# Optimization experiments

Hardware: AMD Instinct MI355X
Metric: run time of the kernel (lower is better)

The kernel has to match this reference:

```python
import jax, jax.numpy as jnp
import numpy as np

GN_GROUPS = 32
GN_EPS = 1e-5


def conv1x1(x, w, b):
    # x: [B,C,H,W], w: [O,C], b: [O]
    return jnp.einsum('bchw,oc->bohw', x, w) + b[None, :, None, None]


def maxpool2(x):
    B, C, H, W = x.shape
    return x.reshape(B, C, H // 2, 2, W // 2, 2).max(axis=(3, 5))


def group_norm(x, w, b, groups=GN_GROUPS, eps=GN_EPS):
    B, C, H, W = x.shape
    xg = x.reshape(B, groups, -1)
    m = xg.mean(axis=-1, keepdims=True)
    v = xg.var(axis=-1, keepdims=True)
    xn = ((xg - m) * jax.lax.rsqrt(v + eps)).reshape(B, C, H, W)
    return xn * w[None, :, None, None] + b[None, :, None, None]


def setup_inputs() -> dict:
    key = jax.random.key(0)
    ks = jax.random.split(key, 8)
    B, C, Ci, H, W = 4, 128, 64, 96, 96
    s_in = 1.0 / np.sqrt(C)
    s_ic = 1.0 / np.sqrt(Ci)
    return {
        'x': jax.random.normal(ks[0], (B, C, H, W), jnp.float32),
        'w_theta': jax.random.normal(ks[1], (Ci, C), jnp.float32) * s_in,
        'b_theta': jnp.zeros((Ci,), jnp.float32),
        'w_phi': jax.random.normal(ks[2], (Ci, C), jnp.float32) * s_in,
        'b_phi': jnp.zeros((Ci,), jnp.float32),
        'w_g': jax.random.normal(ks[3], (Ci, C), jnp.float32) * s_in,
        'b_g': jnp.zeros((Ci,), jnp.float32),
        'w_W': jax.random.normal(ks[4], (C, Ci), jnp.float32) * s_ic,
        'b_W': jnp.zeros((C,), jnp.float32),
        'gn_w': jnp.ones((C,), jnp.float32),
        'gn_b': jnp.zeros((C,), jnp.float32),
    }


def reference(x, w_theta, b_theta, w_phi, b_phi, w_g, b_g, w_W, b_W, gn_w, gn_b):
    B, C, H, W = x.shape
    Ci = w_theta.shape[0]
    # projections (1x1 convs); phi and g are 2x2 max-pooled (sub_sample=True)
    theta = conv1x1(x, w_theta, b_theta).reshape(B, Ci, H * W)          # [B,Ci,N]
    phi = maxpool2(conv1x1(x, w_phi, b_phi)).reshape(B, Ci, -1)         # [B,Ci,N']
    g = maxpool2(conv1x1(x, w_g, b_g)).reshape(B, Ci, -1)               # [B,Ci,N']
    # unscaled single-head attention
    f = jnp.einsum('bcn,bcm->bnm', theta, phi)                          # [B,N,N']
    f = jax.nn.softmax(f, axis=-1)
    y = jnp.einsum('bnm,bcm->bcn', f, g).reshape(B, Ci, H, W)           # [B,Ci,H,W]
    w_y = group_norm(conv1x1(y, w_W, b_W), gn_w, gn_b)
    return w_y + x
```

## Files before the change

kernel.cpp:

```cpp
#include <hip/hip_runtime.h>
#include <math.h>

#define B_ 4
#define C_ 128
#define CI_ 64
#define H_ 96
#define W_ 96
#define HW_ (H_*W_)
#define NP_ 2304
#define GROUPS_ 32
#define EPS_ 1e-5f
#define KVT_ 32
#define NT_ (NP_/KVT_)

typedef _Float16 f16x8 __attribute__((ext_vector_type(8)));
typedef _Float16 f16x2 __attribute__((ext_vector_type(2)));
typedef __attribute__((ext_vector_type(4))) float f32x4;

__device__ inline f32x4 mfma16h(f16x8 a, f16x8 b, f32x4 c) {
    return __builtin_amdgcn_mfma_f32_16x16x32_f16(a, b, c, 0, 0, 0);
}
__device__ inline float h2f(unsigned short s) {
    return (float)__builtin_bit_cast(_Float16, s);
}
__device__ inline unsigned pk_f16(float a, float b) {
    return __builtin_bit_cast(unsigned, __builtin_amdgcn_cvt_pkrtz(a, b));
}
__device__ inline f16x8 pk8(float v0, float v1, float v2, float v3,
                            float v4, float v5, float v6, float v7) {
    uint4 u = { pk_f16(v0, v1), pk_f16(v2, v3), pk_f16(v4, v5), pk_f16(v6, v7) };
    return __builtin_bit_cast(f16x8, u);
}
__device__ inline void gload_lds16(const void* g, void* l) {
    __builtin_amdgcn_global_load_lds(
        (const __attribute__((address_space(1))) void*)reinterpret_cast<uintptr_t>(g),
        (__attribute__((address_space(3))) void*)(unsigned)reinterpret_cast<uintptr_t>(l),
        16, 0, 0);
}

__global__ __launch_bounds__(256) void wprep_kernel(
    const float* __restrict__ w_theta, const float* __restrict__ w_phi,
    const float* __restrict__ w_g,     const float* __restrict__ w_W,
    unsigned short* __restrict__ Whall)
{
    const int idx = blockIdx.x * 256 + threadIdx.x;
    float v;
    if      (idx <  8192) v = w_theta[idx];
    else if (idx < 16384) v = w_phi[idx - 8192];
    else if (idx < 24576) v = w_g[idx - 16384];
    else                  v = w_W[idx - 24576];
    Whall[idx] = __builtin_bit_cast(unsigned short, (_Float16)v);
}

__global__ __launch_bounds__(256) void proj_kernel(
    const float* __restrict__ x, const unsigned short* __restrict__ Whall,
    const float* __restrict__ b_theta, const float* __restrict__ b_phi,
    const float* __restrict__ b_g,
    unsigned short* __restrict__ Qo, unsigned short* __restrict__ phiF,
    unsigned short* __restrict__ gF)
{
    __shared__ __align__(16) unsigned short pb[4][16 * 72];

    const int t    = threadIdx.x;
    const int wv   = t >> 6;
    const int lane = t & 63;
    const int lr   = lane & 15;
    const int lg   = lane >> 4;
    const int b    = blockIdx.y;
    const int px0  = blockIdx.x * 64 + wv * 16;

    const float* xb = x + (size_t)b * C_ * HW_ + px0 + lr;
    f16x8 xa[4];
    #pragma unroll
    for (int u = 0; u < 4; ++u) {
        const float* p = xb + (size_t)(u * 32 + lg * 8) * HW_;
        xa[u] = pk8(p[0], p[(size_t)HW_], p[2 * (size_t)HW_], p[3 * (size_t)HW_],
                    p[4 * (size_t)HW_], p[5 * (size_t)HW_], p[6 * (size_t)HW_],
                    p[7 * (size_t)HW_]);
    }

    #pragma unroll
    for (int mat = 0; mat < 3; ++mat) {
        const unsigned short* Whp = Whall + mat * 8192;
        const float* bsel = (mat == 0) ? b_theta : (mat == 1) ? b_phi : b_g;
        unsigned short* osel = (mat == 0) ? Qo : (mat == 1) ? phiF : gF;

        f32x4 D[4];
        #pragma unroll
        for (int ct = 0; ct < 4; ++ct) D[ct] = (f32x4){0.f, 0.f, 0.f, 0.f};
        #pragma unroll
        for (int u = 0; u < 4; ++u)
            #pragma unroll
            for (int ct = 0; ct < 4; ++ct) {
                f16x8 wb = *(const f16x8*)&Whp[(ct * 16 + lr) * 128 + u * 32 + lg * 8];
                D[ct] = mfma16h(xa[u], wb, D[ct]);
            }

        #pragma unroll
        for (int ct = 0; ct < 4; ++ct) {
            const float bi = bsel[ct * 16 + lr];
            #pragma unroll
            for (int r2 = 0; r2 < 4; ++r2)
                pb[wv][(4 * lg + r2) * 72 + ct * 16 + lr] =
                    __builtin_bit_cast(unsigned short, (_Float16)(D[ct][r2] + bi));
        }
        {
            const int px = lane >> 2, ch = lane & 3;
            f16x8 y0 = *(const f16x8*)&pb[wv][px * 72 + ch * 16];
            f16x8 y1 = *(const f16x8*)&pb[wv][px * 72 + ch * 16 + 8];
            unsigned short* op = osel + ((size_t)b * HW_ + px0 + px) * CI_ + ch * 16;
            *(f16x8*)op       = y0;
            *(f16x8*)(op + 8) = y1;
        }
    }
}

__global__ __launch_bounds__(256) void pool_kernel(
    const unsigned short* __restrict__ phiF, const unsigned short* __restrict__ gF,
    unsigned short* __restrict__ Ko, unsigned short* __restrict__ Vt)
{
    const int t   = threadIdx.x;
    const int b   = blockIdx.y;
    const int mat = blockIdx.z;
    const int idx = blockIdx.x * 256 + t;
    int m, ci;
    if (mat == 0) { m = idx >> 6; ci = idx & 63; }
    else          { ci = idx / NP_; m = idx - ci * NP_; }
    const int ph = m / 48, pw = m % 48;
    const int n00 = (ph * 2) * W_ + pw * 2;
    const unsigned short* src = mat ? gF : phiF;
    const unsigned short* p = src + ((size_t)b * HW_ + n00) * CI_ + ci;
    float v = fmaxf(fmaxf(h2f(p[0]), h2f(p[CI_])),
                    fmaxf(h2f(p[(size_t)W_ * CI_]), h2f(p[(size_t)(W_ + 1) * CI_])));
    unsigned short r = __builtin_bit_cast(unsigned short, (_Float16)v);
    if (mat == 0) {
        Ko[((size_t)b * NP_ + m) * CI_ + ci] = r;
    } else {
        const int ms = (m & ~31) | (8 * ((m >> 2) & 3) + 4 * ((m >> 4) & 1) + (m & 3));
        Vt[((size_t)b * CI_ + ci) * NP_ + ms] = r;
    }
}

__global__ __launch_bounds__(128) void attn_kernel(
    const unsigned short* __restrict__ Qg, const unsigned short* __restrict__ Kg,
    const unsigned short* __restrict__ Vt, unsigned short* __restrict__ Yh)
{
    __shared__ unsigned char Klds[2][4096];
    __shared__ unsigned char Vlds[2][4096];

    const int t    = threadIdx.x;
    const int wv   = t >> 6;
    const int lane = t & 63;
    const int lr   = lane & 15;
    const int lg   = lane >> 4;
    const int b    = blockIdx.y;
    const int q0   = blockIdx.x * 32 + wv * 16;

    const int krow = lane >> 3;
    const int kchk = (lane & 7) ^ krow;
    const int vrow = lane >> 2;
    const int vchk = (lane & 3) ^ (vrow & 3);

    const unsigned short* Kb = Kg + (size_t)b * NP_ * CI_;
    const unsigned short* Vb = Vt + (size_t)b * CI_ * NP_;

    f16x8 qf[2];
    #pragma unroll
    for (int u = 0; u < 2; ++u)
        qf[u] = *(const f16x8*)(Qg + ((size_t)b * HW_ + q0 + lr) * CI_ + u * 32 + lg * 8);

    f32x4 o_acc[4];
    #pragma unroll
    for (int dt = 0; dt < 4; ++dt) o_acc[dt] = (f32x4){0.f, 0.f, 0.f, 0.f};
    float mrun = -1e30f, lrun = 0.f;

#define STAGE(BUF, TT)                                                          \
    {                                                                           \
        const int kv0_ = (TT) * KVT_;                                           \
        if (wv == 0) {                                                          \
            _Pragma("unroll")                                                   \
            for (int i = 0; i < 4; ++i)                                         \
                gload_lds16(Kb + (size_t)(kv0_ + 8 * i + krow) * CI_ + kchk * 8,\
                            &Klds[BUF][i * 1024]);                              \
        } else {                                                                \
            _Pragma("unroll")                                                   \
            for (int i = 0; i < 4; ++i)                                         \
                gload_lds16(Vb + (size_t)(16 * i + vrow) * NP_ + kv0_ + vchk * 8,\
                            &Vlds[BUF][i * 1024]);                              \
        }                                                                       \
    }

#define COMPUTE(BUF)                                                            \
    {                                                                           \
        f16x8 kf[2][2];                                                         \
        _Pragma("unroll")                                                       \
        for (int u = 0; u < 2; ++u)                                             \
            _Pragma("unroll")                                                   \
            for (int k4 = 0; k4 < 2; ++k4)                                      \
                kf[u][k4] = *(const f16x8*)&Klds[BUF][(k4 * 16 + lr) * 128      \
                                + (((4 * u + lg) ^ (lr & 7)) << 4)];            \
        f32x4 s[2];                                                             \
        s[0] = (f32x4){0.f, 0.f, 0.f, 0.f};                                     \
        s[1] = (f32x4){0.f, 0.f, 0.f, 0.f};                                     \
        __builtin_amdgcn_s_setprio(1);                                          \
        _Pragma("unroll")                                                       \
        for (int u = 0; u < 2; ++u) {                                           \
            s[0] = mfma16h(kf[u][0], qf[u], s[0]);                              \
            s[1] = mfma16h(kf[u][1], qf[u], s[1]);                              \
        }                                                                       \
        __builtin_amdgcn_s_setprio(0);                                          \
        float tmax = fmaxf(fmaxf(fmaxf(s[0][0], s[0][1]),                       \
                                 fmaxf(s[0][2], s[0][3])),                      \
                           fmaxf(fmaxf(s[1][0], s[1][1]),                       \
                                 fmaxf(s[1][2], s[1][3])));                     \
        if (!__all(tmax <= mrun + 8.0f)) {                                      \
            tmax = fmaxf(tmax, __shfl_xor(tmax, 16));                           \
            tmax = fmaxf(tmax, __shfl_xor(tmax, 32));                           \
            const float mnew = fmaxf(mrun, tmax);                               \
            const float sc = __expf(mrun - mnew);                               \
            lrun *= sc;                                                         \
            _Pragma("unroll")                                                   \
            for (int r2 = 0; r2 < 4; ++r2) {                                    \
                const float scb = __shfl(sc, 4 * lg + r2);                      \
                _Pragma("unroll")                                               \
                for (int dt = 0; dt < 4; ++dt) o_acc[dt][r2] *= scb;            \
            }                                                                   \
            mrun = mnew;                                                        \
        }                                                                       \
        const float e00 = __expf(s[0][0] - mrun);                               \
        const float e01 = __expf(s[0][1] - mrun);                               \
        const float e02 = __expf(s[0][2] - mrun);                               \
        const float e03 = __expf(s[0][3] - mrun);                               \
        const float e10 = __expf(s[1][0] - mrun);                               \
        const float e11 = __expf(s[1][1] - mrun);                               \
        const float e12 = __expf(s[1][2] - mrun);                               \
        const float e13 = __expf(s[1][3] - mrun);                               \
        lrun += ((e00 + e01) + (e02 + e03)) + ((e10 + e11) + (e12 + e13));      \
        f16x8 pf = pk8(e00, e01, e02, e03, e10, e11, e12, e13);                 \
        __builtin_amdgcn_s_setprio(1);                                          \
        _Pragma("unroll")                                                       \
        for (int dt = 0; dt < 4; ++dt) {                                        \
            const int vrow_ = dt * 16 + lr;                                     \
            f16x8 vf = *(const f16x8*)&Vlds[BUF][vrow_ * 64                     \
                            + (((lg ^ (lr & 3))) << 4)];                        \
            o_acc[dt] = mfma16h(pf, vf, o_acc[dt]);                             \
        }                                                                       \
        __builtin_amdgcn_s_setprio(0);                                          \
    }

    STAGE(0, 0);
    STAGE(1, 1);

    for (int it = 0; it < NT_ / 2; ++it) {
        const int t0 = 2 * it;
        asm volatile("s_waitcnt vmcnt(4)" ::: "memory");
        __builtin_amdgcn_s_barrier();
        COMPUTE(0);
        __builtin_amdgcn_s_barrier();
        if (t0 + 2 < NT_) STAGE(0, t0 + 2);
        if (it == NT_ / 2 - 1) {
            asm volatile("s_waitcnt vmcnt(0)" ::: "memory");
        } else {
            asm volatile("s_waitcnt vmcnt(4)" ::: "memory");
        }
        __builtin_amdgcn_s_barrier();
        COMPUTE(1);
        __builtin_amdgcn_s_barrier();
        if (t0 + 3 < NT_) STAGE(1, t0 + 3);
    }

    float lt = lrun;
    lt += __shfl_xor(lt, 16);
    lt += __shfl_xor(lt, 32);
    unsigned short* yb = (unsigned short*)&Klds[wv][0];
    #pragma unroll
    for (int r2 = 0; r2 < 4; ++r2) {
        const float inv = 1.0f / __shfl(lt, 4 * lg + r2);
        #pragma unroll
        for (int dt = 0; dt < 4; ++dt)
            yb[(4 * lg + r2) * 72 + dt * 16 + lr] =
                __builtin_bit_cast(unsigned short, (_Float16)(o_acc[dt][r2] * inv));
    }
    {
        const int px = lane >> 2, ch = lane & 3;
        f16x8 y0 = *(const f16x8*)&yb[px * 72 + ch * 16];
        f16x8 y1 = *(const f16x8*)&yb[px * 72 + ch * 16 + 8];
        unsigned short* op = Yh + ((size_t)b * HW_ + q0 + px) * CI_ + ch * 16;
        *(f16x8*)op       = y0;
        *(f16x8*)(op + 8) = y1;
    }
#undef STAGE
#undef COMPUTE
}

__global__ __launch_bounds__(256) void conv2_kernel(
    const unsigned short* __restrict__ Yh, const unsigned short* __restrict__ wWh,
    const float* __restrict__ bW, float* __restrict__ Zg, float* __restrict__ gpart)
{
    __shared__ float wpart[4][32][2];

    const int t    = threadIdx.x;
    const int wv   = t >> 6;
    const int lane = t & 63;
    const int lr   = lane & 15;
    const int lg   = lane >> 4;
    const int b    = blockIdx.y;
    const int n0   = blockIdx.x * 64 + wv * 16;

    f16x8 ya[2];
    #pragma unroll
    for (int u = 0; u < 2; ++u)
        ya[u] = *(const f16x8*)(Yh + ((size_t)b * HW_ + n0 + lr) * CI_ + u * 32 + lg * 8);

    float* Zb = Zg + (size_t)b * C_ * HW_ + n0 + lr;
    #pragma unroll
    for (int ot = 0; ot < 8; ++ot) {
        f32x4 D = (f32x4){0.f, 0.f, 0.f, 0.f};
        #pragma unroll
        for (int u = 0; u < 2; ++u) {
            f16x8 wa = *(const f16x8*)&wWh[(ot * 16 + lr) * CI_ + u * 32 + lg * 8];
            D = mfma16h(wa, ya[u], D);
        }
        float zs = 0.f, zq = 0.f;
        #pragma unroll
        for (int r2 = 0; r2 < 4; ++r2) {
            const int o = ot * 16 + 4 * lg + r2;
            const float z = D[r2] + bW[o];
            Zb[(size_t)o * HW_] = z;
            zs += z;
            zq += z * z;
        }
        zs += __shfl_xor(zs, 1);  zq += __shfl_xor(zq, 1);
        zs += __shfl_xor(zs, 2);  zq += __shfl_xor(zq, 2);
        zs += __shfl_xor(zs, 4);  zq += __shfl_xor(zq, 4);
        zs += __shfl_xor(zs, 8);  zq += __shfl_xor(zq, 8);
        if (lr == 0) {
            wpart[wv][ot * 4 + lg][0] = zs;
            wpart[wv][ot * 4 + lg][1] = zq;
        }
    }
    __syncthreads();
    if (t < 64) {
        const int g = t >> 1, w = t & 1;
        const float v = wpart[0][g][w] + wpart[1][g][w]
                      + wpart[2][g][w] + wpart[3][g][w];
        gpart[(((size_t)b * 144 + blockIdx.x) * 32 + g) * 2 + w] = v;
    }
}

__global__ __launch_bounds__(256) void final_kernel(
    const float* __restrict__ Zg, const float* __restrict__ xg,
    const float* __restrict__ gpart, const float* __restrict__ gnw,
    const float* __restrict__ gnb, float* __restrict__ out)
{
    __shared__ float red[256][2];
    const int t = threadIdx.x;
    const int c = blockIdx.x;
    const int b = blockIdx.y;
    const int g = c >> 2;

    float v1 = 0.f, v2 = 0.f;
    if (t < 144) {
        v1 = gpart[(((size_t)b * 144 + t) * 32 + g) * 2 + 0];
        v2 = gpart[(((size_t)b * 144 + t) * 32 + g) * 2 + 1];
    }
    red[t][0] = v1; red[t][1] = v2;
    __syncthreads();
    for (int off = 128; off > 0; off >>= 1) {
        if (t < off) { red[t][0] += red[t + off][0]; red[t][1] += red[t + off][1]; }
        __syncthreads();
    }
    const float invn = 1.0f / (4 * HW_);
    const float mean = red[0][0] * invn;
    const float var  = red[0][1] * invn - mean * mean;
    const float rstd = rsqrtf(var + EPS_);
    const float sc = rstd * gnw[c];
    const float sh = gnb[c] - mean * sc;

    const float4* zp = (const float4*)(Zg + ((size_t)b * C_ + c) * HW_);
    const float4* xp = (const float4*)(xg + ((size_t)b * C_ + c) * HW_);
    float4*       op = (float4*)(out + ((size_t)b * C_ + c) * HW_);
    #pragma unroll
    for (int i = 0; i < HW_ / 4 / 256; ++i) {
        const int j = i * 256 + t;
        const float4 z  = zp[j];
        const float4 xv = xp[j];
        float4 o;
        o.x = z.x * sc + sh + xv.x;
        o.y = z.y * sc + sh + xv.y;
        o.z = z.z * sc + sh + xv.z;
        o.w = z.w * sc + sh + xv.w;
        op[j] = o;
    }
}

extern "C" void kernel_launch(void* const* d_in, const int* in_sizes, int n_in,
                              void* d_out, int out_size, void* d_ws, size_t ws_size,
                              hipStream_t stream)
{
    const float* x       = (const float*)d_in[0];
    const float* w_theta = (const float*)d_in[1];
    const float* b_theta = (const float*)d_in[2];
    const float* w_phi   = (const float*)d_in[3];
    const float* b_phi   = (const float*)d_in[4];
    const float* w_g     = (const float*)d_in[5];
    const float* b_g     = (const float*)d_in[6];
    const float* w_W     = (const float*)d_in[7];
    const float* b_W     = (const float*)d_in[8];
    const float* gn_w    = (const float*)d_in[9];
    const float* gn_b    = (const float*)d_in[10];
    float* out = (float*)d_out;
    char* wsb  = (char*)d_ws;

    unsigned short* Q    = (unsigned short*)(wsb);
    unsigned short* K    = (unsigned short*)(wsb +  4718592);
    unsigned short* Vt   = (unsigned short*)(wsb +  5898240);
    unsigned short* phiF = (unsigned short*)(wsb +  7077888);
    unsigned short* gF   = (unsigned short*)(wsb + 11796480);
    unsigned short* Yh   = (unsigned short*)(wsb +  7077888);
    float* gpart         = (float*)(wsb + 11796480);
    float* Z             = (float*)(wsb + 16515072);
    unsigned short* Whall= (unsigned short*)(wsb + 35390464);
    unsigned short* wWh  = Whall + 24576;

    wprep_kernel<<<128, 256, 0, stream>>>(w_theta, w_phi, w_g, w_W, Whall);
    proj_kernel <<<dim3(HW_ / 64, B_), 256, 0, stream>>>(
        x, Whall, b_theta, b_phi, b_g, Q, phiF, gF);
    pool_kernel <<<dim3(NP_ * CI_ / 256, B_, 2), 256, 0, stream>>>(phiF, gF, K, Vt);
    attn_kernel <<<dim3(HW_ / 32, B_), 128, 0, stream>>>(Q, K, Vt, Yh);
    conv2_kernel<<<dim3(HW_ / 64, B_), 256, 0, stream>>>(Yh, wWh, b_W, Z, gpart);
    final_kernel<<<dim3(C_, B_), 256, 0, stream>>>(Z, x, gpart, gn_w, gn_b, out);
}
```

Before: 117.0 us.

## Store conv2 output as fp16, fuse pooling passes, and shrink blocks for more parallelism

```diff
diff --git a/kernel.cpp b/kernel.cpp
--- a/kernel.cpp
+++ b/kernel.cpp
@@ -12,6 +12,7 @@
 #define EPS_ 1e-5f
 #define KVT_ 32
 #define NT_ (NP_/KVT_)
+#define NBLK_ 288
 
 typedef _Float16 f16x8 __attribute__((ext_vector_type(8)));
 typedef _Float16 f16x2 __attribute__((ext_vector_type(2)));
@@ -52,14 +53,14 @@
     Whall[idx] = __builtin_bit_cast(unsigned short, (_Float16)v);
 }
 
-__global__ __launch_bounds__(256) void proj_kernel(
+__global__ __launch_bounds__(128) void proj_kernel(
     const float* __restrict__ x, const unsigned short* __restrict__ Whall,
     const float* __restrict__ b_theta, const float* __restrict__ b_phi,
     const float* __restrict__ b_g,
     unsigned short* __restrict__ Qo, unsigned short* __restrict__ phiF,
     unsigned short* __restrict__ gF)
 {
-    __shared__ __align__(16) unsigned short pb[4][16 * 72];
+    __shared__ __align__(16) unsigned short pb[2][16 * 72];
 
     const int t    = threadIdx.x;
     const int wv   = t >> 6;
@@ -67,7 +68,7 @@
     const int lr   = lane & 15;
     const int lg   = lane >> 4;
     const int b    = blockIdx.y;
-    const int px0  = blockIdx.x * 64 + wv * 16;
+    const int px0  = blockIdx.x * 32 + wv * 16;
 
     const float* xb = x + (size_t)b * C_ * HW_ + px0 + lr;
     f16x8 xa[4];
@@ -119,25 +120,39 @@
     const unsigned short* __restrict__ phiF, const unsigned short* __restrict__ gF,
     unsigned short* __restrict__ Ko, unsigned short* __restrict__ Vt)
 {
-    const int t   = threadIdx.x;
-    const int b   = blockIdx.y;
-    const int mat = blockIdx.z;
-    const int idx = blockIdx.x * 256 + t;
-    int m, ci;
-    if (mat == 0) { m = idx >> 6; ci = idx & 63; }
-    else          { ci = idx / NP_; m = idx - ci * NP_; }
-    const int ph = m / 48, pw = m % 48;
-    const int n00 = (ph * 2) * W_ + pw * 2;
-    const unsigned short* src = mat ? gF : phiF;
-    const unsigned short* p = src + ((size_t)b * HW_ + n00) * CI_ + ci;
-    float v = fmaxf(fmaxf(h2f(p[0]), h2f(p[CI_])),
-                    fmaxf(h2f(p[(size_t)W_ * CI_]), h2f(p[(size_t)(W_ + 1) * CI_])));
-    unsigned short r = __builtin_bit_cast(unsigned short, (_Float16)v);
-    if (mat == 0) {
-        Ko[((size_t)b * NP_ + m) * CI_ + ci] = r;
-    } else {
-        const int ms = (m & ~31) | (8 * ((m >> 2) & 3) + 4 * ((m >> 4) & 1) + (m & 3));
-        Vt[((size_t)b * CI_ + ci) * NP_ + ms] = r;
+    __shared__ unsigned short vbuf[32][66];
+    const int t  = threadIdx.x;
+    const int b  = blockIdx.y;
+    const int m0 = blockIdx.x * 32;
+
+    {
+        const int ci = t & 63;
+        #pragma unroll
+        for (int i = 0; i < 8; ++i) {
+            const int ml = (t >> 6) + 4 * i;
+            const int m  = m0 + ml;
+            const int ph = m / 48, pw = m % 48;
+            const size_t base = ((size_t)b * HW_ + (ph * 2) * W_ + pw * 2) * CI_ + ci;
+            const unsigned short* pk_ = phiF + base;
+            const unsigned short* pg_ = gF + base;
+            float kv = fmaxf(fmaxf(h2f(pk_[0]), h2f(pk_[CI_])),
+                             fmaxf(h2f(pk_[(size_t)W_ * CI_]), h2f(pk_[(size_t)(W_ + 1) * CI_])));
+            float gv = fmaxf(fmaxf(h2f(pg_[0]), h2f(pg_[CI_])),
+                             fmaxf(h2f(pg_[(size_t)W_ * CI_]), h2f(pg_[(size_t)(W_ + 1) * CI_])));
+            Ko[((size_t)b * NP_ + m) * CI_ + ci] =
+                __builtin_bit_cast(unsigned short, (_Float16)kv);
+            vbuf[ml][ci] = __builtin_bit_cast(unsigned short, (_Float16)gv);
+        }
+    }
+    __syncthreads();
+    {
+        const int ml = t & 31;
+        const int ms = (8 * ((ml >> 2) & 3) + 4 * ((ml >> 4) & 1) + (ml & 3));
+        #pragma unroll
+        for (int i = 0; i < 8; ++i) {
+            const int ci = (t >> 5) + 8 * i;
+            Vt[((size_t)b * CI_ + ci) * NP_ + m0 + ms] = vbuf[ml][ci];
+        }
     }
 }
 
@@ -293,11 +308,12 @@
 #undef COMPUTE
 }
 
-__global__ __launch_bounds__(256) void conv2_kernel(
+__global__ __launch_bounds__(128) void conv2_kernel(
     const unsigned short* __restrict__ Yh, const unsigned short* __restrict__ wWh,
-    const float* __restrict__ bW, float* __restrict__ Zg, float* __restrict__ gpart)
-{
-    __shared__ float wpart[4][32][2];
+    const float* __restrict__ bW, unsigned short* __restrict__ Zh,
+    float* __restrict__ gpart)
+{
+    __shared__ float wpart[2][32][2];
 
     const int t    = threadIdx.x;
     const int wv   = t >> 6;
@@ -305,14 +321,14 @@
     const int lr   = lane & 15;
     const int lg   = lane >> 4;
     const int b    = blockIdx.y;
-    const int n0   = blockIdx.x * 64 + wv * 16;
+    const int n0   = blockIdx.x * 32 + wv * 16;
 
     f16x8 ya[2];
     #pragma unroll
     for (int u = 0; u < 2; ++u)
         ya[u] = *(const f16x8*)(Yh + ((size_t)b * HW_ + n0 + lr) * CI_ + u * 32 + lg * 8);
 
-    float* Zb = Zg + (size_t)b * C_ * HW_ + n0 + lr;
+    unsigned short* Zb = Zh + (size_t)b * C_ * HW_ + n0 + lr;
     #pragma unroll
     for (int ot = 0; ot < 8; ++ot) {
         f32x4 D = (f32x4){0.f, 0.f, 0.f, 0.f};
@@ -326,7 +342,7 @@
         for (int r2 = 0; r2 < 4; ++r2) {
             const int o = ot * 16 + 4 * lg + r2;
             const float z = D[r2] + bW[o];
-            Zb[(size_t)o * HW_] = z;
+            Zb[(size_t)o * HW_] = __builtin_bit_cast(unsigned short, (_Float16)z);
             zs += z;
             zq += z * z;
         }
@@ -342,14 +358,13 @@
     __syncthreads();
     if (t < 64) {
         const int g = t >> 1, w = t & 1;
-        const float v = wpart[0][g][w] + wpart[1][g][w]
-                      + wpart[2][g][w] + wpart[3][g][w];
-        gpart[(((size_t)b * 144 + blockIdx.x) * 32 + g) * 2 + w] = v;
+        const float v = wpart[0][g][w] + wpart[1][g][w];
+        gpart[(((size_t)b * NBLK_ + blockIdx.x) * 32 + g) * 2 + w] = v;
     }
 }
 
 __global__ __launch_bounds__(256) void final_kernel(
-    const float* __restrict__ Zg, const float* __restrict__ xg,
+    const unsigned short* __restrict__ Zh, const float* __restrict__ xg,
     const float* __restrict__ gpart, const float* __restrict__ gnw,
     const float* __restrict__ gnb, float* __restrict__ out)
 {
@@ -357,12 +372,13 @@
     const int t = threadIdx.x;
     const int c = blockIdx.x;
     const int b = blockIdx.y;
+    const int zc = blockIdx.z;
     const int g = c >> 2;
 
     float v1 = 0.f, v2 = 0.f;
-    if (t < 144) {
-        v1 = gpart[(((size_t)b * 144 + t) * 32 + g) * 2 + 0];
-        v2 = gpart[(((size_t)b * 144 + t) * 32 + g) * 2 + 1];
+    for (int j = t; j < NBLK_; j += 256) {
+        v1 += gpart[(((size_t)b * NBLK_ + j) * 32 + g) * 2 + 0];
+        v2 += gpart[(((size_t)b * NBLK_ + j) * 32 + g) * 2 + 1];
     }
     red[t][0] = v1; red[t][1] = v2;
     __syncthreads();
@@ -377,19 +393,19 @@
     const float sc = rstd * gnw[c];
     const float sh = gnb[c] - mean * sc;
 
-    const float4* zp = (const float4*)(Zg + ((size_t)b * C_ + c) * HW_);
+    const unsigned short* zp = Zh + ((size_t)b * C_ + c) * HW_;
     const float4* xp = (const float4*)(xg + ((size_t)b * C_ + c) * HW_);
     float4*       op = (float4*)(out + ((size_t)b * C_ + c) * HW_);
     #pragma unroll
-    for (int i = 0; i < HW_ / 4 / 256; ++i) {
-        const int j = i * 256 + t;
-        const float4 z  = zp[j];
+    for (int i = 0; i < 3; ++i) {
+        const int j = (zc * 3 + i) * 256 + t;
+        const ushort4 zv = *(const ushort4*)(zp + (size_t)j * 4);
         const float4 xv = xp[j];
         float4 o;
-        o.x = z.x * sc + sh + xv.x;
-        o.y = z.y * sc + sh + xv.y;
-        o.z = z.z * sc + sh + xv.z;
-        o.w = z.w * sc + sh + xv.w;
+        o.x = h2f(zv.x) * sc + sh + xv.x;
+        o.y = h2f(zv.y) * sc + sh + xv.y;
+        o.z = h2f(zv.z) * sc + sh + xv.z;
+        o.w = h2f(zv.w) * sc + sh + xv.w;
         op[j] = o;
     }
 }
@@ -419,15 +435,15 @@
     unsigned short* gF   = (unsigned short*)(wsb + 11796480);
     unsigned short* Yh   = (unsigned short*)(wsb +  7077888);
     float* gpart         = (float*)(wsb + 11796480);
-    float* Z             = (float*)(wsb + 16515072);
+    unsigned short* Zh   = (unsigned short*)(wsb + 16515072);
     unsigned short* Whall= (unsigned short*)(wsb + 35390464);
     unsigned short* wWh  = Whall + 24576;
 
     wprep_kernel<<<128, 256, 0, stream>>>(w_theta, w_phi, w_g, w_W, Whall);
-    proj_kernel <<<dim3(HW_ / 64, B_), 256, 0, stream>>>(
+    proj_kernel <<<dim3(NBLK_, B_), 128, 0, stream>>>(
         x, Whall, b_theta, b_phi, b_g, Q, phiF, gF);
-    pool_kernel <<<dim3(NP_ * CI_ / 256, B_, 2), 256, 0, stream>>>(phiF, gF, K, Vt);
+    pool_kernel <<<dim3(NP_ / 32, B_), 256, 0, stream>>>(phiF, gF, K, Vt);
     attn_kernel <<<dim3(HW_ / 32, B_), 128, 0, stream>>>(Q, K, Vt, Yh);
-    conv2_kernel<<<dim3(HW_ / 64, B_), 256, 0, stream>>>(Yh, wWh, b_W, Z, gpart);
-    final_kernel<<<dim3(C_, B_), 256, 0, stream>>>(Z, x, gpart, gn_w, gn_b, out);
-}
+    conv2_kernel<<<dim3(NBLK_, B_), 128, 0, stream>>>(Yh, wWh, b_W, Zh, gpart);
+    final_kernel<<<dim3(C_, B_, 3), 256, 0, stream>>>(Zh, x, gpart, gn_w, gn_b, out);
+}
```

After: 104.3 us. -10.9%, faster.
